# Optimization experiments

Measured on AMD Instinct MI355X. Metric: run time of the kernel, lower is better.

## Reference

```python
import jax, jax.numpy as jnp
import numpy as np

B, N, G = 32, 262144, 256


def setup_inputs() -> dict:
    key = jax.random.key(0)
    k1, k2, k3 = jax.random.split(key, 3)
    pr = jax.random.normal(k1, (B, N), dtype=jnp.float32)
    inp_means = jax.random.normal(k2, (B, G), dtype=jnp.float32)
    vr = jax.random.randint(k3, (B, N, 1), 0, G, dtype=jnp.int32)
    W = jnp.ones((2,), dtype=jnp.float32)  # hist_weight, ones initializer
    return {"pr": pr, "inp_means": inp_means, "vr": vr, "W": W}


def reference(pr, inp_means, vr, W):
    sg = jax.lax.stop_gradient
    G = inp_means.shape[1]
    v = jnp.squeeze(vr, -1)  # [B, N] int cluster ids (stop_gradient in orig; int anyway)
    p_sg = sg(pr)

    # Per-batch segmented min/max/sum/any over clusters (replaces python loop over g).
    def seg(p, psg, vi):
        mn = jnp.full((G,), jnp.inf, p.dtype).at[vi].min(psg)    # min(where(gidx, pr, inf))
        mx = jnp.full((G,), -jnp.inf, p.dtype).at[vi].max(psg)   # max(where(gidx, pr, -inf))
        sm = jnp.zeros((G,), p.dtype).at[vi].add(p)              # sum(where(gidx, pr, 0))
        any_ = jnp.zeros((G,), bool).at[vi].set(True)            # reduce_any(gidx)
        return mn, mx, sm, any_

    vmins, vmaxs, vsum, vany = jax.vmap(seg)(pr, p_sg, v)  # each [B, G]
    # Original divides sum by cast(any)->1.0 (or 0/0=nan -> 0), i.e. the group SUM.
    vmeans = jnp.where(vany, vsum, jnp.zeros((), pr.dtype))
    vmeans = (inp_means * W[0] + vmeans * W[1]) / (W[0] + W[1])

    no_scale = vmins == vmaxs  # [B, G]
    vmins_g = jnp.take_along_axis(jnp.where(no_scale, 0.0, vmins), v, axis=1)  # [B, N]
    vmaxs_g = jnp.take_along_axis(jnp.where(no_scale, 1.0, vmaxs), v, axis=1)  # [B, N]

    sort_ids = jnp.argsort(vmeans, axis=1)
    orig_ids = jnp.argsort(sort_ids, axis=1)  # inverse permutation
    vs = jnp.take_along_axis(vmeans, sort_ids, axis=1)  # [B, G]
    cd = jnp.concatenate([vs[:, :1], vs, vs[:, -1:] * 2], axis=1)  # [B, G+2]
    # conv1d with kernel ones(2)/c, VALID: out[i] = (cd[i] + cd[i+1]) / c
    f0 = (cd[:, :-2] + cd[:, 1:-1]) / 1.999  # conv(...)[:, :-1]
    f1 = (cd[:, 1:-1] + cd[:, 2:]) / 2.001   # conv(...)[:, 1:]
    f0 = jnp.take_along_axis(
        jnp.where(no_scale, 0.0, jnp.take_along_axis(f0, orig_ids, axis=1)), v, axis=1)
    f1 = jnp.take_along_axis(
        jnp.where(no_scale, 1.0, jnp.take_along_axis(f1, orig_ids, axis=1)), v, axis=1)

    tmp = (sg(pr) - sg(vmins_g)) / sg(vmaxs_g - vmins_g) * (f1 - f0) + f0  # [B, N]
    bad = jnp.isnan(tmp) | (tmp == 0.0)
    s = pr / jnp.where(bad, 1.0, tmp)  # safe denominator (grad-safe)
    scale = jnp.where(bad | jnp.isnan(s) | jnp.isinf(s), 0.0, s)
    return pr * scale
```

## Files before the change

kernel.cpp:

```cpp
#include <hip/hip_runtime.h>
#include <math.h>

#define NB 32
#define NN 262144
#define NG 256
#define NC 64
#define CH (NN/NC)
#define SC (CH/4)
#define CD 64
#define ELD (NN/CD)
#define LCAP 1536

__global__ __launch_bounds__(256) void k_count(const int* __restrict__ vr,
                                               unsigned* __restrict__ cnt){
  __shared__ unsigned scnt[NG];
  const int t = threadIdx.x;
  scnt[t] = 0u;
  __syncthreads();

  const int b = blockIdx.x / NC;
  const int c = blockIdx.x % NC;
  const size_t base = (size_t)b*NN + (size_t)c*CH;
  const int4* v4 = (const int4*)(vr + base);

#pragma unroll
  for (int i = 0; i < CH/1024; i++){
    int4 v = v4[i*256 + t];
    atomicAdd(&scnt[v.x], 1u);
    atomicAdd(&scnt[v.y], 1u);
    atomicAdd(&scnt[v.z], 1u);
    atomicAdd(&scnt[v.w], 1u);
  }
  __syncthreads();
  cnt[(size_t)(b*NC + c)*NG + t] = scnt[t];
}

__global__ __launch_bounds__(256) void k_offsets(unsigned* __restrict__ cnt,
                                                 unsigned* __restrict__ grpbase,
                                                 unsigned* __restrict__ grplen){
  const int b = blockIdx.x;
  const int g = threadIdx.x;
  unsigned tot = 0;
#pragma unroll 8
  for (int c = 0; c < NC; c++) tot += cnt[(size_t)(b*NC + c)*NG + g];

  __shared__ unsigned ss[NG];
  ss[g] = tot; __syncthreads();
  for (int d = 1; d < NG; d <<= 1){
    unsigned v = (g >= d) ? ss[g - d] : 0u;
    __syncthreads();
    ss[g] += v;
    __syncthreads();
  }
  unsigned base = ss[g] - tot;

  unsigned run = base;
  for (int c = 0; c < NC; c++){
    size_t idx = (size_t)(b*NC + c)*NG + g;
    unsigned x = cnt[idx];
    cnt[idx] = run;
    run += x;
  }
  grpbase[b*NG + g] = base;
  grplen [b*NG + g] = tot;
}

__global__ __launch_bounds__(256) void k_scatter(const float* __restrict__ pr,
                                                 const int* __restrict__ vr,
                                                 const unsigned* __restrict__ off,
                                                 float* __restrict__ sorted){
  __shared__ float vbuf[CH];
  __shared__ unsigned graw32[CH/4];
  __shared__ unsigned char gbuf[CH];
  __shared__ unsigned wcnt[4][NG];
  __shared__ unsigned bias[NG];
  __shared__ unsigned ss[NG];
  const int t    = threadIdx.x;
  const int lane = t & 63;
  const int w    = t >> 6;
  const int b = blockIdx.x / NC;
  const int c = blockIdx.x % NC;
  const size_t base = (size_t)b*NN + (size_t)c*CH;

#pragma unroll
  for (int k = 0; k < 4; k++) wcnt[k][t] = 0u;
  __syncthreads();

  {
    const int4* v4 = (const int4*)(vr + base + (size_t)w*SC);
#pragma unroll
    for (int i = 0; i < SC/256; i++){
      int4 v = v4[i*64 + lane];
      atomicAdd(&wcnt[w][v.x], 1u);
      atomicAdd(&wcnt[w][v.y], 1u);
      atomicAdd(&wcnt[w][v.z], 1u);
      atomicAdd(&wcnt[w][v.w], 1u);
      graw32[w*(SC/4) + i*64 + lane] =
        (unsigned)v.x | ((unsigned)v.y << 8) | ((unsigned)v.z << 16) | ((unsigned)v.w << 24);
    }
  }
  __syncthreads();

  {
    unsigned c0 = wcnt[0][t], c1 = wcnt[1][t], c2 = wcnt[2][t], c3 = wcnt[3][t];
    unsigned tot = c0 + c1 + c2 + c3;
    ss[t] = tot; __syncthreads();
    for (int d = 1; d < NG; d <<= 1){
      unsigned v = (t >= d) ? ss[t - d] : 0u;
      __syncthreads();
      ss[t] += v;
      __syncthreads();
    }
    unsigned lb = ss[t] - tot;
    wcnt[0][t] = lb;
    wcnt[1][t] = lb + c0;
    wcnt[2][t] = lb + c0 + c1;
    wcnt[3][t] = lb + c0 + c1 + c2;
    bias[t] = off[(size_t)(b*NC + c)*NG + t] - lb;
  }
  __syncthreads();

  {
    const unsigned long long below = (lane == 0) ? 0ull : ((1ull << lane) - 1ull);
    const float* psrc = pr + base + (size_t)w*SC;
    const int shft = (lane & 3) * 8;
    for (int s = 0; s < SC/64; s++){
      float p = psrc[s*64 + lane];
      unsigned packed = graw32[w*(SC/4) + s*16 + (lane >> 2)];
      int g = (int)((packed >> shft) & 255u);
      unsigned long long mask = ~0ull;
#pragma unroll
      for (int bit = 0; bit < 8; bit++){
        int bv = (g >> bit) & 1;
        unsigned long long bal = __ballot(bv);
        mask &= bv ? bal : ~bal;
      }
      int rank = __popcll(mask & below);
      unsigned old = wcnt[w][g];
      if (rank == 0) wcnt[w][g] = old + (unsigned)__popcll(mask);
      vbuf[old + (unsigned)rank] = p;
      gbuf[old + (unsigned)rank] = (unsigned char)g;
    }
  }
  __syncthreads();

  {
    float* dst = sorted + (size_t)b*NN;
    const unsigned* gbuf32 = (const unsigned*)gbuf;
#pragma unroll
    for (int k = 0; k < CH/256; k++){
      int p = k*256 + t;
      unsigned packed = gbuf32[p >> 2];
      unsigned g = (packed >> ((p & 3) * 8)) & 255u;
      dst[bias[g] + (unsigned)p] = vbuf[p];
    }
  }
}

__global__ __launch_bounds__(64) void k_sum(const float* __restrict__ sorted,
                                            const unsigned* __restrict__ grpbase,
                                            const unsigned* __restrict__ grplen,
                                            float* __restrict__ gsum,
                                            float* __restrict__ gmn,
                                            float* __restrict__ gmx){
  __shared__ float4 sm4[LCAP/4];
  float* sm = (float*)sm4;
  const int lane = threadIdx.x;
  const int b = blockIdx.x / NG;
  const int g = blockIdx.x % NG;

  const unsigned base = grpbase[b*NG + g];
  const unsigned len  = grplen [b*NG + g];
  const float* src = sorted + (size_t)b*NN + base;

  float mn = INFINITY, mx = -INFINITY;
  for (unsigned i = lane; i < len; i += 64){
    float v = src[i];
    mn = fminf(mn, v);
    mx = fmaxf(mx, v);
    if (i < LCAP) sm[i] = v;
  }
#pragma unroll
  for (int d = 32; d > 0; d >>= 1){
    mn = fminf(mn, __shfl_down(mn, d));
    mx = fmaxf(mx, __shfl_down(mx, d));
  }
  __syncthreads();

  if (lane == 0){
    const unsigned lim = (len < LCAP) ? len : LCAP;
    float s = 0.0f;
    unsigned i = 0;
    for (; i + 8 <= lim; i += 8){
      float4 a = sm4[i/4], c = sm4[i/4 + 1];
      s = __fadd_rn(s, a.x); s = __fadd_rn(s, a.y);
      s = __fadd_rn(s, a.z); s = __fadd_rn(s, a.w);
      s = __fadd_rn(s, c.x); s = __fadd_rn(s, c.y);
      s = __fadd_rn(s, c.z); s = __fadd_rn(s, c.w);
    }
    for (; i < lim; i++) s = __fadd_rn(s, sm[i]);
    for (unsigned j = lim; j < len; j++) s = __fadd_rn(s, src[j]);
    gsum[b*NG + g] = s;
    gmn [b*NG + g] = mn;
    gmx [b*NG + g] = mx;
  }
}

__global__ __launch_bounds__(256) void k_pipeline(const float* __restrict__ gsum,
                                                  const float* __restrict__ gmn,
                                                  const float* __restrict__ gmx,
                                                  const float* __restrict__ inp_means,
                                                  const float* __restrict__ Wv,
                                                  float4* __restrict__ params){
  const int b = blockIdx.x;
  const int g = threadIdx.x;
  __shared__ float vm[NG];
  __shared__ float vs[NG];

  const float s   = gsum[b*NG + g];
  const float mnf = gmn [b*NG + g];
  const float mxf = gmx [b*NG + g];
  const float W0 = Wv[0], W1 = Wv[1];
  float mean = __fdiv_rn(__fadd_rn(__fmul_rn(inp_means[b*NG + g], W0),
                                   __fmul_rn(s, W1)),
                         __fadd_rn(W0, W1));
  vm[g] = mean;
  __syncthreads();

  int r = 0;
  for (int j = 0; j < NG; j++){
    float x = vm[j];
    r += (x < mean) || (x == mean && j < g);
  }
  vs[r] = mean;
  __syncthreads();

  float c0 = (r == 0)    ? vs[0]                     : vs[r-1];
  float c1 = vs[r];
  float c2 = (r == NG-1) ? __fmul_rn(vs[NG-1], 2.0f) : vs[r+1];
  float f0 = __fdiv_rn(__fadd_rn(c0, c1), 1.999f);
  float f1 = __fdiv_rn(__fadd_rn(c1, c2), 2.001f);

  bool ns = (mnf == mxf);
  float4 q;
  q.x = ns ? 0.0f : mnf;
  q.y = ns ? 1.0f : __fsub_rn(mxf, mnf);
  q.z = ns ? 1.0f : __fsub_rn(f1, f0);
  q.w = ns ? 0.0f : f0;
  params[b*NG + g] = q;
}

static __device__ __forceinline__ float apply_one(float p, int g, const float4* __restrict__ sp){
  float4 q = sp[g];
  float t1  = __fsub_rn(p, q.x);
  float t3  = __fdiv_rn(t1, q.y);
  float t5  = __fmul_rn(t3, q.z);
  float tmp = __fadd_rn(t5, q.w);
  bool bad = __builtin_isnan(tmp) || (tmp == 0.0f);
  float s = __fdiv_rn(p, bad ? 1.0f : tmp);
  bool bad2 = bad || __builtin_isnan(s) || __builtin_isinf(s);
  float sc = bad2 ? 0.0f : s;
  return __fmul_rn(p, sc);
}

__global__ __launch_bounds__(256) void k_apply(const float* __restrict__ pr,
                                               const int* __restrict__ vr,
                                               const float4* __restrict__ params,
                                               float* __restrict__ out){
  __shared__ float4 sp[NG];
  const int t = threadIdx.x;
  const int b = blockIdx.x / CD;
  const int c = blockIdx.x % CD;

  sp[t] = params[b*NG + t];
  __syncthreads();

  const size_t base = (size_t)b*NN + (size_t)c*ELD;
  const float4* p4 = (const float4*)(pr + base);
  const int4*  v4 = (const int4*)(vr + base);
  float4* o4 = (float4*)(out + base);

#pragma unroll
  for (int i = 0; i < ELD/1024; i++){
    float4 p = p4[i*256 + t];
    int4   v = v4[i*256 + t];
    float4 r;
    r.x = apply_one(p.x, v.x, sp);
    r.y = apply_one(p.y, v.y, sp);
    r.z = apply_one(p.z, v.z, sp);
    r.w = apply_one(p.w, v.w, sp);
    o4[i*256 + t] = r;
  }
}

extern "C" void kernel_launch(void* const* d_in, const int* in_sizes, int n_in,
                              void* d_out, int out_size, void* d_ws, size_t ws_size,
                              hipStream_t stream){
  const float* pr        = (const float*)d_in[0];
  const float* inp_means = (const float*)d_in[1];
  const int*   vr        = (const int*)d_in[2];
  const float* W         = (const float*)d_in[3];
  float* out = (float*)d_out;

  char* ws = (char*)d_ws;
  size_t o = 0;
  unsigned* cnt     = (unsigned*)(ws + o); o += (size_t)NB*NC*NG*4;
  unsigned* grpbase = (unsigned*)(ws + o); o += (size_t)NB*NG*4;
  unsigned* grplen  = (unsigned*)(ws + o); o += (size_t)NB*NG*4;
  float*    gsum    = (float*)   (ws + o); o += (size_t)NB*NG*4;
  float*    gmn     = (float*)   (ws + o); o += (size_t)NB*NG*4;
  float*    gmx     = (float*)   (ws + o); o += (size_t)NB*NG*4;
  float4*   params  = (float4*)  (ws + o); o += (size_t)NB*NG*16;
  float* sorted = out;

  k_count   <<<NB*NC, 256, 0, stream>>>(vr, cnt);
  k_offsets <<<NB,     NG, 0, stream>>>(cnt, grpbase, grplen);
  k_scatter <<<NB*NC, 256, 0, stream>>>(pr, vr, cnt, sorted);
  k_sum     <<<NB*NG,  64, 0, stream>>>(sorted, grpbase, grplen, gsum, gmn, gmx);
  k_pipeline<<<NB,     NG, 0, stream>>>(gsum, gmn, gmx, inp_means, W, params);
  k_apply   <<<NB*CD, 256, 0, stream>>>(pr, vr, params, out);
}
```

Measured before the change: 197.0 us.

## Compute per-group sum/min/max with one thread per group instead of one wavefront

The group reduction kernel now assigns each cluster to a single thread, which serially sums, mins and maxes its contiguous segment. This removes the shared-memory staging, shuffle reduction and barrier, and shrinks the launch from one 64-thread block per group to 128 blocks total. Each thread now walks roughly a thousand elements with strided, uncoalesced loads across lanes, and only 8192 threads are active. That low parallelism risks exposing memory latency compared with the earlier per-group wavefront cooperation.

```diff
diff --git a/kernel.cpp b/kernel.cpp
--- a/kernel.cpp
+++ b/kernel.cpp
@@ -9,7 +9,6 @@
 #define SC (CH/4)
 #define CD 64
 #define ELD (NN/CD)
-#define LCAP 1536
 
 __global__ __launch_bounds__(256) void k_count(const int* __restrict__ vr,
                                                unsigned* __restrict__ cnt){
@@ -163,47 +162,38 @@
                                             float* __restrict__ gsum,
                                             float* __restrict__ gmn,
                                             float* __restrict__ gmx){
-  __shared__ float4 sm4[LCAP/4];
-  float* sm = (float*)sm4;
   const int lane = threadIdx.x;
-  const int b = blockIdx.x / NG;
-  const int g = blockIdx.x % NG;
+  const int b = blockIdx.x >> 2;
+  const int g = ((blockIdx.x & 3) << 6) + lane;
 
   const unsigned base = grpbase[b*NG + g];
   const unsigned len  = grplen [b*NG + g];
   const float* src = sorted + (size_t)b*NN + base;
 
-  float mn = INFINITY, mx = -INFINITY;
-  for (unsigned i = lane; i < len; i += 64){
+  float s = 0.0f, mn = INFINITY, mx = -INFINITY;
+  unsigned i = 0;
+  const unsigned n8 = len & ~7u;
+  for (; i < n8; i += 8){
+    float v0 = src[i+0], v1 = src[i+1], v2 = src[i+2], v3 = src[i+3];
+    float v4 = src[i+4], v5 = src[i+5], v6 = src[i+6], v7 = src[i+7];
+    s = __fadd_rn(s, v0); s = __fadd_rn(s, v1);
+    s = __fadd_rn(s, v2); s = __fadd_rn(s, v3);
+    s = __fadd_rn(s, v4); s = __fadd_rn(s, v5);
+    s = __fadd_rn(s, v6); s = __fadd_rn(s, v7);
+    mn = fminf(mn, fminf(fminf(v0, v1), fminf(v2, v3)));
+    mn = fminf(mn, fminf(fminf(v4, v5), fminf(v6, v7)));
+    mx = fmaxf(mx, fmaxf(fmaxf(v0, v1), fmaxf(v2, v3)));
+    mx = fmaxf(mx, fmaxf(fmaxf(v4, v5), fmaxf(v6, v7)));
+  }
+  for (; i < len; i++){
     float v = src[i];
+    s = __fadd_rn(s, v);
     mn = fminf(mn, v);
     mx = fmaxf(mx, v);
-    if (i < LCAP) sm[i] = v;
-  }
-#pragma unroll
-  for (int d = 32; d > 0; d >>= 1){
-    mn = fminf(mn, __shfl_down(mn, d));
-    mx = fmaxf(mx, __shfl_down(mx, d));
-  }
-  __syncthreads();
-
-  if (lane == 0){
-    const unsigned lim = (len < LCAP) ? len : LCAP;
-    float s = 0.0f;
-    unsigned i = 0;
-    for (; i + 8 <= lim; i += 8){
-      float4 a = sm4[i/4], c = sm4[i/4 + 1];
-      s = __fadd_rn(s, a.x); s = __fadd_rn(s, a.y);
-      s = __fadd_rn(s, a.z); s = __fadd_rn(s, a.w);
-      s = __fadd_rn(s, c.x); s = __fadd_rn(s, c.y);
-      s = __fadd_rn(s, c.z); s = __fadd_rn(s, c.w);
-    }
-    for (; i < lim; i++) s = __fadd_rn(s, sm[i]);
-    for (unsigned j = lim; j < len; j++) s = __fadd_rn(s, src[j]);
-    gsum[b*NG + g] = s;
-    gmn [b*NG + g] = mn;
-    gmx [b*NG + g] = mx;
-  }
+  }
+  gsum[b*NG + g] = s;
+  gmn [b*NG + g] = mn;
+  gmx [b*NG + g] = mx;
 }
 
 __global__ __launch_bounds__(256) void k_pipeline(const float* __restrict__ gsum,
@@ -316,7 +306,7 @@
   k_count   <<<NB*NC, 256, 0, stream>>>(vr, cnt);
   k_offsets <<<NB,     NG, 0, stream>>>(cnt, grpbase, grplen);
   k_scatter <<<NB*NC, 256, 0, stream>>>(pr, vr, cnt, sorted);
-  k_sum     <<<NB*NG,  64, 0, stream>>>(sorted, grpbase, grplen, gsum, gmn, gmx);
+  k_sum     <<<NB*4,   64, 0, stream>>>(sorted, grpbase, grplen, gsum, gmn, gmx);
   k_pipeline<<<NB,     NG, 0, stream>>>(gsum, gmn, gmx, inp_means, W, params);
   k_apply   <<<NB*CD, 256, 0, stream>>>(pr, vr, params, out);
 }
```

After: 215.1 us. +9.2%, slower.
